# Kernel optimization log

Measured on AMD Instinct MI355X. Metric: run time of the kernel, lower is better.

Reference implementation:

```python
import jax, jax.numpy as jnp
import numpy as np

TOP_K = 8
N_GROUP = 8
TOPK_GROUP = 4
ROUTED_SCALING_FACTOR = 2.5
NORM_TOPK_PROB = True
TOKENS = 16384
HIDDEN = 4096
N_EXPERTS = 256


def setup_inputs() -> dict:
    key = jax.random.key(0)
    k1, k2, k3 = jax.random.split(key, 3)
    x = jax.random.normal(k1, (TOKENS, HIDDEN), dtype=jnp.float32)
    weight = jax.random.normal(k2, (N_EXPERTS, HIDDEN), dtype=jnp.float32) * 0.02
    e_score_correction_bias = jax.random.normal(k3, (N_EXPERTS,), dtype=jnp.float32) * 0.01
    return {"x": x, "weight": weight, "e_score_correction_bias": e_score_correction_bias}


def reference(x, weight, e_score_correction_bias):
    # gates: [T, E]
    gates = x @ weight.T
    orig_scores = jax.nn.sigmoid(gates.astype(jnp.float32))
    scores = orig_scores + e_score_correction_bias
    T, E = scores.shape
    eg = E // N_GROUP  # experts per group
    s = scores.reshape(T, N_GROUP, eg)
    # group score = sum of top-2 expert scores within each group -> [T, G]
    group_scores = jax.lax.top_k(s, 2)[0].sum(axis=-1)
    # torch code selects the (n_group - topk_group) SMALLEST groups and keeps
    # only those (masked_fill zeroes everything else) -- replicate faithfully.
    k_drop = N_GROUP - TOPK_GROUP
    _, bottom_idx = jax.lax.top_k(-group_scores, k_drop)  # [T, k_drop]
    keep = jnp.zeros((T, N_GROUP), dtype=bool).at[jnp.arange(T)[:, None], bottom_idx].set(True)
    s = jnp.where(keep[:, :, None], s, 0.0).reshape(T, E)
    # torch.topk(-scores) -> indices of the k SMALLEST scores
    _, inds = jax.lax.top_k(-s, TOP_K)  # [T, top_k]
    sel = jnp.take_along_axis(orig_scores, inds, axis=-1)
    if TOP_K > 1 and NORM_TOPK_PROB:
        sel = sel / (sel.sum(axis=-1, keepdims=True) + 1e-20)
    sel = sel * ROUTED_SCALING_FACTOR
    return inds, sel
```

## Files before the change

### kernel.cpp

```cpp
#include <hip/hip_runtime.h>
#include <hip/hip_fp16.h>
#include <cstdint>
#include <cmath>

#define TOKENS  16384
#define HIDDEN  4096
#define NEXP    256
#define TOPK    8
#define KDROP   4

typedef _Float16 f16x8  __attribute__((ext_vector_type(8)));
typedef float    f32x16 __attribute__((ext_vector_type(16)));

#define LO_SCALE 2048.0f
#define LO_INV   (1.0f/2048.0f)

#define WS_G0_OFF 0
#define WS_G1_OFF 16777216
#define WS_WH_OFF 33554432
#define WS_WL_OFF 35651584

__global__ __launch_bounds__(256)
void wsplit(const float* __restrict__ w, _Float16* __restrict__ wh,
            _Float16* __restrict__ wl)
{
    const int idx = blockIdx.x * 256 + threadIdx.x;
    const int e   = idx >> 9;
    const int kg8 = idx & 511;
    const float4* p = (const float4*)(w + (size_t)e * HIDDEN + kg8 * 8);
    float4 f0 = p[0], f1 = p[1];
    float v[8] = {f0.x, f0.y, f0.z, f0.w, f1.x, f1.y, f1.z, f1.w};
    f16x8 hi, lo;
    #pragma unroll
    for (int i = 0; i < 8; ++i) {
        _Float16 h = (_Float16)v[i];
        hi[i] = h;
        lo[i] = (_Float16)((v[i] - (float)h) * LO_SCALE);
    }
    const int kc = kg8 >> 2, s = (kg8 >> 1) & 1, hl = kg8 & 1;
    const int cid = ((kc * 2 + s) * 8 + (e >> 5)) * 64 + hl * 32 + (e & 31);
    ((f16x8*)wh)[cid] = hi;
    ((f16x8*)wl)[cid] = lo;
}

__global__ __launch_bounds__(256, 2)
void gemm_split(const float* __restrict__ x, const _Float16* __restrict__ wh,
                const _Float16* __restrict__ wl,
                float* __restrict__ g0, float* __restrict__ g1)
{
    __shared__ _Float16 Ah[2][64 * 32];
    __shared__ _Float16 Al[2][64 * 32];

    const int tid  = threadIdx.x;
    const int wv   = tid >> 6;
    const int lane = tid & 63;
    const int tok0 = blockIdx.x * 64;
    const int kcg0 = blockIdx.y * 64;
    float* gates_half = blockIdx.y ? g1 : g0;

    const int sm = tid >> 2;
    const int sq = tid & 3;
    const float* xr = x + (size_t)(tok0 + sm) * HIDDEN;
    const int scid = ((sq >> 1) * 2 + (sm >> 5)) * 64 + (sq & 1) * 32 + (sm & 31);

    const f16x8* whc = (const f16x8*)wh;
    const f16x8* wlc = (const f16x8*)wl;

    f32x16 accH[2][2] = {};
    f32x16 accX[2][2] = {};

    f16x8 bh[2][2], bl[2][2];

    {
        const float4* ap = (const float4*)(xr + kcg0 * 32 + sq * 8);
        float4 f0 = ap[0];
        float4 f1 = ap[1];
        #pragma unroll
        for (int s = 0; s < 2; ++s) {
            const int base = ((kcg0 * 2 + s) * 8 + wv * 2) * 64 + lane;
            bh[s][0] = whc[base];
            bh[s][1] = whc[base + 64];
            bl[s][0] = wlc[base];
            bl[s][1] = wlc[base + 64];
        }
        float v[8] = {f0.x, f0.y, f0.z, f0.w, f1.x, f1.y, f1.z, f1.w};
        f16x8 hi, lo;
        #pragma unroll
        for (int i = 0; i < 8; ++i) {
            _Float16 h = (_Float16)v[i];
            hi[i] = h;
            lo[i] = (_Float16)((v[i] - (float)h) * LO_SCALE);
        }
        *(f16x8*)&Ah[0][scid * 8] = hi;
        *(f16x8*)&Al[0][scid * 8] = lo;
    }
    __syncthreads();

    #pragma unroll 2
    for (int kc = 0; kc < 64; ++kc) {
        const int cur  = kc & 1;
        const bool more = (kc < 63);

        float4 a0n, a1n;
        f16x8 bhn[2][2], bln[2][2];
        if (more) {
            const int kcg = kcg0 + kc + 1;
            const float4* ap = (const float4*)(xr + kcg * 32 + sq * 8);
            a0n = ap[0];
            a1n = ap[1];
            #pragma unroll
            for (int s = 0; s < 2; ++s) {
                const int base = ((kcg * 2 + s) * 8 + wv * 2) * 64 + lane;
                bhn[s][0] = whc[base];
                bhn[s][1] = whc[base + 64];
                bln[s][0] = wlc[base];
                bln[s][1] = wlc[base + 64];
            }
        }

        #pragma unroll
        for (int s = 0; s < 2; ++s) {
            f16x8 ah0 = *(const f16x8*)&Ah[cur][((s * 2 + 0) * 64 + lane) * 8];
            f16x8 ah1 = *(const f16x8*)&Ah[cur][((s * 2 + 1) * 64 + lane) * 8];
            f16x8 al0 = *(const f16x8*)&Al[cur][((s * 2 + 0) * 64 + lane) * 8];
            f16x8 al1 = *(const f16x8*)&Al[cur][((s * 2 + 1) * 64 + lane) * 8];

            accH[0][0] = __builtin_amdgcn_mfma_f32_32x32x16_f16(ah0, bh[s][0], accH[0][0], 0, 0, 0);
            accH[0][1] = __builtin_amdgcn_mfma_f32_32x32x16_f16(ah0, bh[s][1], accH[0][1], 0, 0, 0);
            accH[1][0] = __builtin_amdgcn_mfma_f32_32x32x16_f16(ah1, bh[s][0], accH[1][0], 0, 0, 0);
            accH[1][1] = __builtin_amdgcn_mfma_f32_32x32x16_f16(ah1, bh[s][1], accH[1][1], 0, 0, 0);
            accX[0][0] = __builtin_amdgcn_mfma_f32_32x32x16_f16(al0, bh[s][0], accX[0][0], 0, 0, 0);
            accX[0][1] = __builtin_amdgcn_mfma_f32_32x32x16_f16(al0, bh[s][1], accX[0][1], 0, 0, 0);
            accX[1][0] = __builtin_amdgcn_mfma_f32_32x32x16_f16(al1, bh[s][0], accX[1][0], 0, 0, 0);
            accX[1][1] = __builtin_amdgcn_mfma_f32_32x32x16_f16(al1, bh[s][1], accX[1][1], 0, 0, 0);
            accX[0][0] = __builtin_amdgcn_mfma_f32_32x32x16_f16(ah0, bl[s][0], accX[0][0], 0, 0, 0);
            accX[0][1] = __builtin_amdgcn_mfma_f32_32x32x16_f16(ah0, bl[s][1], accX[0][1], 0, 0, 0);
            accX[1][0] = __builtin_amdgcn_mfma_f32_32x32x16_f16(ah1, bl[s][0], accX[1][0], 0, 0, 0);
            accX[1][1] = __builtin_amdgcn_mfma_f32_32x32x16_f16(ah1, bl[s][1], accX[1][1], 0, 0, 0);
        }

        if (more) {
            float v[8] = {a0n.x, a0n.y, a0n.z, a0n.w, a1n.x, a1n.y, a1n.z, a1n.w};
            f16x8 hi, lo;
            #pragma unroll
            for (int i = 0; i < 8; ++i) {
                _Float16 h = (_Float16)v[i];
                hi[i] = h;
                lo[i] = (_Float16)((v[i] - (float)h) * LO_SCALE);
            }
            *(f16x8*)&Ah[cur ^ 1][scid * 8] = hi;
            *(f16x8*)&Al[cur ^ 1][scid * 8] = lo;
            #pragma unroll
            for (int s = 0; s < 2; ++s) {
                bh[s][0] = bhn[s][0]; bh[s][1] = bhn[s][1];
                bl[s][0] = bln[s][0]; bl[s][1] = bln[s][1];
            }
        }
        __syncthreads();
    }

    const int col   = lane & 31;
    const int rbase = 4 * (lane >> 5);
    #pragma unroll
    for (int r = 0; r < 2; ++r)
        #pragma unroll
        for (int c = 0; c < 2; ++c) {
            float* gp = gates_half + (size_t)(tok0 + r * 32) * NEXP + wv * 64 + c * 32 + col;
            #pragma unroll
            for (int reg = 0; reg < 16; ++reg) {
                const int row = (reg & 3) + 8 * (reg >> 2) + rbase;
                gp[(size_t)row * NEXP] = accH[r][c][reg] + accX[r][c][reg] * LO_INV;
            }
        }
}

__device__ __forceinline__ unsigned ordkey(float f) {
    unsigned u = __float_as_uint(f);
    return (u & 0x80000000u) ? ~u : (u | 0x80000000u);
}

__global__ __launch_bounds__(256, 4)
void gate_epilogue(const float* __restrict__ g0,
                   const float* __restrict__ g1,
                   const float* __restrict__ bias,
                   float* __restrict__ out)
{
    const int tid  = threadIdx.x;
    const int wv   = tid >> 6;
    const int lane = tid & 63;
    const int t    = blockIdx.x * 4 + wv;

    float4 ga = ((const float4*)(g0 + (size_t)t * NEXP))[lane];
    float4 gb = ((const float4*)(g1 + (size_t)t * NEXP))[lane];
    float4 bv = ((const float4*)bias)[lane];
    float4 gv = make_float4(ga.x + gb.x, ga.y + gb.y, ga.z + gb.z, ga.w + gb.w);

    float sig0 = 1.0f / (1.0f + expf(-gv.x));
    float sig1 = 1.0f / (1.0f + expf(-gv.y));
    float sig2 = 1.0f / (1.0f + expf(-gv.z));
    float sig3 = 1.0f / (1.0f + expf(-gv.w));
    float sc0 = sig0 + bv.x, sc1 = sig1 + bv.y;
    float sc2 = sig2 + bv.z, sc3 = sig3 + bv.w;

    float m1 = fmaxf(sc0, sc1);
    float m2 = fminf(sc0, sc1);
    if (sc2 > m1) { m2 = m1; m1 = sc2; } else m2 = fmaxf(m2, sc2);
    if (sc3 > m1) { m2 = m1; m1 = sc3; } else m2 = fmaxf(m2, sc3);
    #pragma unroll
    for (int off = 1; off < 8; off <<= 1) {
        float o1 = __shfl_xor(m1, off);
        float o2 = __shfl_xor(m2, off);
        float nm1 = fmaxf(m1, o1);
        float nm2 = fmaxf(fminf(m1, o1), fmaxf(m2, o2));
        m1 = nm1; m2 = nm2;
    }
    float gsum = m1 + m2;
    float gs[8];
    #pragma unroll
    for (int gi = 0; gi < 8; ++gi) gs[gi] = __shfl(gsum, gi * 8);

    int keepmask = 0;
    #pragma unroll
    for (int g = 0; g < 8; ++g) {
        int rank = 0;
        #pragma unroll
        for (int h = 0; h < 8; ++h)
            rank += (gs[h] < gs[g]) || (gs[h] == gs[g] && h < g);
        if (rank < KDROP) keepmask |= (1 << g);
    }
    const bool kept = (keepmask >> (lane >> 3)) & 1;

    const unsigned ib = (unsigned)(lane * 4);
    unsigned long long k0 = ((unsigned long long)ordkey(kept ? sc0 : 0.0f) << 32) | (ib + 0);
    unsigned long long k1 = ((unsigned long long)ordkey(kept ? sc1 : 0.0f) << 32) | (ib + 1);
    unsigned long long k2 = ((unsigned long long)ordkey(kept ? sc2 : 0.0f) << 32) | (ib + 2);
    unsigned long long k3 = ((unsigned long long)ordkey(kept ? sc3 : 0.0f) << 32) | (ib + 3);

    float ssum = 0.0f, myval = 0.0f;
    int myidx = 0;
    #pragma unroll
    for (int r = 0; r < TOPK; ++r) {
        unsigned long long kmin = k0 < k1 ? k0 : k1;
        if (k2 < kmin) kmin = k2;
        if (k3 < kmin) kmin = k3;
        #pragma unroll
        for (int off = 32; off >= 1; off >>= 1) {
            unsigned long long o = __shfl_xor(kmin, off);
            if (o < kmin) kmin = o;
        }
        const int id   = (int)(kmin & 0xffffffffull);
        const int src  = id >> 2;
        const int slot = id & 3;
        float vsrc = (slot == 0) ? sig0 : (slot == 1) ? sig1
                   : (slot == 2) ? sig2 : sig3;
        float v = __shfl(vsrc, src);
        ssum += v;
        if (lane == r) { myidx = id; myval = v; }
        const bool mine = (lane == src);
        if (mine && slot == 0) k0 = ~0ull;
        if (mine && slot == 1) k1 = ~0ull;
        if (mine && slot == 2) k2 = ~0ull;
        if (mine && slot == 3) k3 = ~0ull;
    }

    if (lane < TOPK) {
        out[(size_t)t * TOPK + lane] = (float)myidx;
        out[(size_t)TOKENS * TOPK + (size_t)t * TOPK + lane] =
            myval / (ssum + 1e-20f) * 2.5f;
    }
}

extern "C" void kernel_launch(void* const* d_in, const int* in_sizes, int n_in,
                              void* d_out, int out_size, void* d_ws, size_t ws_size,
                              hipStream_t stream)
{
    const float* x    = (const float*)d_in[0];
    const float* w    = (const float*)d_in[1];
    const float* bias = (const float*)d_in[2];
    float* out = (float*)d_out;

    float*     g0 = (float*)((char*)d_ws + WS_G0_OFF);
    float*     g1 = (float*)((char*)d_ws + WS_G1_OFF);
    _Float16*  wh = (_Float16*)((char*)d_ws + WS_WH_OFF);
    _Float16*  wl = (_Float16*)((char*)d_ws + WS_WL_OFF);

    wsplit<<<dim3(512), dim3(256), 0, stream>>>(w, wh, wl);
    gemm_split<<<dim3(TOKENS / 64, 2), dim3(256), 0, stream>>>(x, wh, wl, g0, g1);
    gate_epilogue<<<dim3(TOKENS / 4), dim3(256), 0, stream>>>(g0, g1, bias, out);
}
```

Before: 431.3 us.

## Double token tile per GEMM block and prefetch activations two chunks ahead

New measurement: 567.4 us. +31.6%, slower.

```diff
diff --git a/kernel.cpp b/kernel.cpp
--- a/kernel.cpp
+++ b/kernel.cpp
@@ -43,41 +43,50 @@
     ((f16x8*)wl)[cid] = lo;
 }
 
-__global__ __launch_bounds__(256, 2)
+__global__ __launch_bounds__(256, 1)
 void gemm_split(const float* __restrict__ x, const _Float16* __restrict__ wh,
                 const _Float16* __restrict__ wl,
                 float* __restrict__ g0, float* __restrict__ g1)
 {
-    __shared__ _Float16 Ah[2][64 * 32];
-    __shared__ _Float16 Al[2][64 * 32];
+    __shared__ _Float16 Ah[2][128 * 32];
+    __shared__ _Float16 Al[2][128 * 32];
 
     const int tid  = threadIdx.x;
     const int wv   = tid >> 6;
     const int lane = tid & 63;
-    const int tok0 = blockIdx.x * 64;
+    const int tok0 = blockIdx.x * 128;
     const int kcg0 = blockIdx.y * 64;
     float* gates_half = blockIdx.y ? g1 : g0;
 
-    const int sm = tid >> 2;
-    const int sq = tid & 3;
-    const float* xr = x + (size_t)(tok0 + sm) * HIDDEN;
-    const int scid = ((sq >> 1) * 2 + (sm >> 5)) * 64 + (sq & 1) * 32 + (sm & 31);
+    const int sr = tid >> 1;
+    const int sp = tid & 1;
+    const float* xr = x + (size_t)(tok0 + sr) * HIDDEN + sp * 16;
+    const int mt_s   = sr >> 5;
+    const int m_s    = sr & 31;
+    const int scid0 = ((sp * 4) + mt_s) * 64 + 0 * 32 + m_s + (sp ? 0 : 0);
+    const int scidA = (sp * 4 + mt_s) * 64 + m_s;
+    const int scidB = scidA + 32;
 
     const f16x8* whc = (const f16x8*)wh;
     const f16x8* wlc = (const f16x8*)wl;
 
-    f32x16 accH[2][2] = {};
-    f32x16 accX[2][2] = {};
+    f32x16 accH[4][2] = {};
+    f32x16 accX[4][2] = {};
 
     f16x8 bh[2][2], bl[2][2];
+    float4 ar[4];
 
     {
-        const float4* ap = (const float4*)(xr + kcg0 * 32 + sq * 8);
-        float4 f0 = ap[0];
-        float4 f1 = ap[1];
+        const float4* ap0 = (const float4*)(xr + (size_t)kcg0 * 32);
+        float4 f0 = ap0[0], f1 = ap0[1];
+        const float4* ap1 = (const float4*)(xr + (size_t)(kcg0 + 1) * 32);
+        ar[0] = ap1[0]; ar[1] = ap1[1];
+        ar[2] = ap1[0]; ar[3] = ap1[1];
+        ar[0] = ap1[0]; ar[1] = ap1[1];
+
         #pragma unroll
         for (int s = 0; s < 2; ++s) {
-            const int base = ((kcg0 * 2 + s) * 8 + wv * 2) * 64 + lane;
+            const int base = (((size_t)0 + kcg0) * 2 + s) * 8 * 64 + wv * 2 * 64 + lane;
             bh[s][0] = whc[base];
             bh[s][1] = whc[base + 64];
             bl[s][0] = wlc[base];
@@ -91,23 +100,41 @@
             hi[i] = h;
             lo[i] = (_Float16)((v[i] - (float)h) * LO_SCALE);
         }
-        *(f16x8*)&Ah[0][scid * 8] = hi;
-        *(f16x8*)&Al[0][scid * 8] = lo;
+        *(f16x8*)&Ah[0][scidA * 8] = *(f16x8*)&hi;
+        f16x8 hiA, loA, hiB, loB;
+        #pragma unroll
+        for (int i = 0; i < 8; ++i) { hiA[i] = hi[i]; loA[i] = lo[i]; }
+        *(f16x8*)&Ah[0][scidA * 8] = hiA;
+        *(f16x8*)&Al[0][scidA * 8] = loA;
+        float v2[8] = {0,0,0,0,0,0,0,0};
+        const float4* ap0b = ap0 + 2;
+        float4 f2 = ap0b[0], f3 = ap0b[1];
+        float vb[8] = {f2.x, f2.y, f2.z, f2.w, f3.x, f3.y, f3.z, f3.w};
+        #pragma unroll
+        for (int i = 0; i < 8; ++i) {
+            _Float16 h = (_Float16)vb[i];
+            hiB[i] = h;
+            loB[i] = (_Float16)((vb[i] - (float)h) * LO_SCALE);
+        }
+        *(f16x8*)&Ah[0][scidB * 8] = hiB;
+        *(f16x8*)&Al[0][scidB * 8] = loB;
+        (void)v2;
+        ar[0] = ap1[0]; ar[1] = ap1[1]; ar[2] = ap1[2]; ar[3] = ap1[3];
     }
     __syncthreads();
 
     #pragma unroll 2
     for (int kc = 0; kc < 64; ++kc) {
-        const int cur  = kc & 1;
-        const bool more = (kc < 63);
-
-        float4 a0n, a1n;
+        const int cur = kc & 1;
+
+        float4 arn[4];
         f16x8 bhn[2][2], bln[2][2];
-        if (more) {
+        if (kc < 62) {
+            const float4* ap = (const float4*)(xr + (size_t)(kcg0 + kc + 2) * 32);
+            arn[0] = ap[0]; arn[1] = ap[1]; arn[2] = ap[2]; arn[3] = ap[3];
+        }
+        if (kc < 63) {
             const int kcg = kcg0 + kc + 1;
-            const float4* ap = (const float4*)(xr + kcg * 32 + sq * 8);
-            a0n = ap[0];
-            a1n = ap[1];
             #pragma unroll
             for (int s = 0; s < 2; ++s) {
                 const int base = ((kcg * 2 + s) * 8 + wv * 2) * 64 + lane;
@@ -120,36 +147,44 @@
 
         #pragma unroll
         for (int s = 0; s < 2; ++s) {
-            f16x8 ah0 = *(const f16x8*)&Ah[cur][((s * 2 + 0) * 64 + lane) * 8];
-            f16x8 ah1 = *(const f16x8*)&Ah[cur][((s * 2 + 1) * 64 + lane) * 8];
-            f16x8 al0 = *(const f16x8*)&Al[cur][((s * 2 + 0) * 64 + lane) * 8];
-            f16x8 al1 = *(const f16x8*)&Al[cur][((s * 2 + 1) * 64 + lane) * 8];
-
-            accH[0][0] = __builtin_amdgcn_mfma_f32_32x32x16_f16(ah0, bh[s][0], accH[0][0], 0, 0, 0);
-            accH[0][1] = __builtin_amdgcn_mfma_f32_32x32x16_f16(ah0, bh[s][1], accH[0][1], 0, 0, 0);
-            accH[1][0] = __builtin_amdgcn_mfma_f32_32x32x16_f16(ah1, bh[s][0], accH[1][0], 0, 0, 0);
-            accH[1][1] = __builtin_amdgcn_mfma_f32_32x32x16_f16(ah1, bh[s][1], accH[1][1], 0, 0, 0);
-            accX[0][0] = __builtin_amdgcn_mfma_f32_32x32x16_f16(al0, bh[s][0], accX[0][0], 0, 0, 0);
-            accX[0][1] = __builtin_amdgcn_mfma_f32_32x32x16_f16(al0, bh[s][1], accX[0][1], 0, 0, 0);
-            accX[1][0] = __builtin_amdgcn_mfma_f32_32x32x16_f16(al1, bh[s][0], accX[1][0], 0, 0, 0);
-            accX[1][1] = __builtin_amdgcn_mfma_f32_32x32x16_f16(al1, bh[s][1], accX[1][1], 0, 0, 0);
-            accX[0][0] = __builtin_amdgcn_mfma_f32_32x32x16_f16(ah0, bl[s][0], accX[0][0], 0, 0, 0);
-            accX[0][1] = __builtin_amdgcn_mfma_f32_32x32x16_f16(ah0, bl[s][1], accX[0][1], 0, 0, 0);
-            accX[1][0] = __builtin_amdgcn_mfma_f32_32x32x16_f16(ah1, bl[s][0], accX[1][0], 0, 0, 0);
-            accX[1][1] = __builtin_amdgcn_mfma_f32_32x32x16_f16(ah1, bl[s][1], accX[1][1], 0, 0, 0);
-        }
-
-        if (more) {
-            float v[8] = {a0n.x, a0n.y, a0n.z, a0n.w, a1n.x, a1n.y, a1n.z, a1n.w};
-            f16x8 hi, lo;
+            f16x8 ah[4], al[4];
+            #pragma unroll
+            for (int mt = 0; mt < 4; ++mt) {
+                ah[mt] = *(const f16x8*)&Ah[cur][((s * 4 + mt) * 64 + lane) * 8];
+                al[mt] = *(const f16x8*)&Al[cur][((s * 4 + mt) * 64 + lane) * 8];
+            }
+            #pragma unroll
+            for (int mt = 0; mt < 4; ++mt) {
+                #pragma unroll
+                for (int c = 0; c < 2; ++c) {
+                    accH[mt][c] = __builtin_amdgcn_mfma_f32_32x32x16_f16(ah[mt], bh[s][c], accH[mt][c], 0, 0, 0);
+                    accX[mt][c] = __builtin_amdgcn_mfma_f32_32x32x16_f16(al[mt], bh[s][c], accX[mt][c], 0, 0, 0);
+                    accX[mt][c] = __builtin_amdgcn_mfma_f32_32x32x16_f16(ah[mt], bl[s][c], accX[mt][c], 0, 0, 0);
+                }
+            }
+        }
+
+        if (kc < 63) {
+            float va[8] = {ar[0].x, ar[0].y, ar[0].z, ar[0].w,
+                           ar[1].x, ar[1].y, ar[1].z, ar[1].w};
+            float vb[8] = {ar[2].x, ar[2].y, ar[2].z, ar[2].w,
+                           ar[3].x, ar[3].y, ar[3].z, ar[3].w};
+            f16x8 hiA, loA, hiB, loB;
             #pragma unroll
             for (int i = 0; i < 8; ++i) {
-                _Float16 h = (_Float16)v[i];
-                hi[i] = h;
-                lo[i] = (_Float16)((v[i] - (float)h) * LO_SCALE);
-            }
-            *(f16x8*)&Ah[cur ^ 1][scid * 8] = hi;
-            *(f16x8*)&Al[cur ^ 1][scid * 8] = lo;
+                _Float16 hA = (_Float16)va[i];
+                hiA[i] = hA;
+                loA[i] = (_Float16)((va[i] - (float)hA) * LO_SCALE);
+                _Float16 hB = (_Float16)vb[i];
+                hiB[i] = hB;
+                loB[i] = (_Float16)((vb[i] - (float)hB) * LO_SCALE);
+            }
+            *(f16x8*)&Ah[cur ^ 1][scidA * 8] = hiA;
+            *(f16x8*)&Al[cur ^ 1][scidA * 8] = loA;
+            *(f16x8*)&Ah[cur ^ 1][scidB * 8] = hiB;
+            *(f16x8*)&Al[cur ^ 1][scidB * 8] = loB;
+            #pragma unroll
+            for (int i = 0; i < 4; ++i) ar[i] = arn[i];
             #pragma unroll
             for (int s = 0; s < 2; ++s) {
                 bh[s][0] = bhn[s][0]; bh[s][1] = bhn[s][1];
@@ -162,14 +197,14 @@
     const int col   = lane & 31;
     const int rbase = 4 * (lane >> 5);
     #pragma unroll
-    for (int r = 0; r < 2; ++r)
+    for (int mt = 0; mt < 4; ++mt)
         #pragma unroll
         for (int c = 0; c < 2; ++c) {
-            float* gp = gates_half + (size_t)(tok0 + r * 32) * NEXP + wv * 64 + c * 32 + col;
+            float* gp = gates_half + (size_t)(tok0 + mt * 32) * NEXP + wv * 64 + c * 32 + col;
             #pragma unroll
             for (int reg = 0; reg < 16; ++reg) {
                 const int row = (reg & 3) + 8 * (reg >> 2) + rbase;
-                gp[(size_t)row * NEXP] = accH[r][c][reg] + accX[r][c][reg] * LO_INV;
+                gp[(size_t)row * NEXP] = accH[mt][c][reg] + accX[mt][c][reg] * LO_INV;
             }
         }
 }
@@ -285,6 +320,6 @@
     _Float16*  wl = (_Float16*)((char*)d_ws + WS_WL_OFF);
 
     wsplit<<<dim3(512), dim3(256), 0, stream>>>(w, wh, wl);
-    gemm_split<<<dim3(TOKENS / 64, 2), dim3(256), 0, stream>>>(x, wh, wl, g0, g1);
+    gemm_split<<<dim3(TOKENS / 128, 2), dim3(256), 0, stream>>>(x, wh, wl, g0, g1);
     gate_epilogue<<<dim3(TOKENS / 4), dim3(256), 0, stream>>>(g0, g1, bias, out);
 }
```
